# Optimization experiments

Measured on AMD Instinct MI355X. Metric: run time of the kernel, lower is better.

The kernel has to match this reference:

```python
import jax, jax.numpy as jnp
import numpy as np


def setup_inputs() -> dict:
    key = jax.random.key(0)
    ks = jax.random.split(key, 8)
    B, L, U, D = 256, 16, 512, 2
    x = jax.random.randint(ks[0], (B, L, L), 0, D, dtype=jnp.int32)
    def s(k, shape, fan):
        return jax.random.normal(k, shape, jnp.float32) / np.float32(np.sqrt(fan))
    return {
        "x": x,
        "W_in_h": s(ks[1], (D, U), D),
        "W_in_v": s(ks[2], (D, U), D),
        "W_carry_h": s(ks[3], (U, U), U),
        "b_carry_h": jnp.zeros((U,), jnp.float32),
        "W_carry_v": s(ks[4], (U, U), U),
        "W_out": s(ks[5], (U, D), U),
        "b_out": jnp.zeros((D,), jnp.float32),
    }


def reference(x, W_in_h, W_in_v, W_carry_h, b_carry_h, W_carry_v, W_out, b_out):
    B, L = x.shape[0], x.shape[1]
    U = W_carry_h.shape[0]
    D = W_out.shape[1]

    # one-hot spins, padded: zero row above, zero columns left/right
    oh = jax.nn.one_hot(jnp.transpose(x, (1, 2, 0)), D, dtype=jnp.float32)  # (L,L,B,D)
    inputs = jnp.zeros((L + 1, L + 2, B, D), jnp.float32).at[1:, 1:-1].set(oh)
    direction = jnp.where(jnp.arange(L) % 2 == 0, 1, -1)  # boustrophedon row flips

    def rev(line, d):
        return jnp.where(d == 1, line, jnp.flip(line, 0))

    def cell(h, xs):
        xh, xv, cv = xs  # left one-hot (B,D), above one-hot (B,D), above hidden (B,U)
        new = jax.nn.elu(xh @ W_in_h + xv @ W_in_v + h @ W_carry_h + b_carry_h + cv @ W_carry_v)
        p = jax.nn.softmax(new @ W_out + b_out)  # (B,D)
        return new, (new, p)

    def row(states, xs):
        cur, prev, d = xs  # (L+2,B,D), (L+2,B,D), scalar direction
        cur_r, prev_r, st_r = rev(cur, d), rev(prev, d), rev(states, d)
        _, (new_states, probs) = jax.lax.scan(
            cell, jnp.zeros((B, U), jnp.float32),
            (cur_r[:-2], prev_r[1:-1], st_r))
        logp = jnp.log(jnp.sum(probs * cur_r[1:-1], axis=2))  # (L,B)
        return rev(new_states, d), jnp.sum(logp, axis=0)

    _, prob = jax.lax.scan(row, jnp.zeros((L, B, U), jnp.float32),
                           (inputs[1:], inputs[:-1], direction))
    return jnp.nan_to_num(jnp.sum(prob, axis=0))  # (B,) log-probabilities
```

## Files before the change

kernel.cpp:

```cpp
#include <hip/hip_runtime.h>
#include <hip/hip_bf16.h>
#include <math.h>

#define Bsz 256
#define Lsz 16
#define Usz 512
#define BPW 2
#define NWG (Bsz / BPW)
#define NT  512

typedef __attribute__((ext_vector_type(8))) short bf16x8;
typedef __attribute__((ext_vector_type(4))) float f32x4;

__device__ __forceinline__ unsigned short f2bf(float f) {
    union { __hip_bfloat16 h; unsigned short s; } u;
    u.h = __float2bfloat16(f);
    return u.s;
}

__device__ __forceinline__ int st_off(int row, int k) {
    return row * Usz + ((k & 504) ^ ((row & 7) << 3)) + (k & 7);
}

__global__ void conv_wch_k(const float* __restrict__ W, unsigned int* __restrict__ out) {
    int j = blockIdx.x * 256 + threadIdx.x;
    float2 w = *(const float2*)(W + 2 * (size_t)j);
    out[j] = (unsigned)f2bf(w.x) | ((unsigned)f2bf(w.y) << 16);
}

__global__ void conv_wcv_k(const float* __restrict__ W, unsigned int* __restrict__ out) {
    int tile = blockIdx.x;
    int l    = threadIdx.x;
    int kb = tile >> 5, ub = tile & 31;
    int k0 = kb * 32 + (l >> 4) * 8;
    int u  = ub * 16 + (l & 15);
    unsigned v[4];
    #pragma unroll
    for (int p = 0; p < 4; ++p) {
        unsigned lo = f2bf(W[(size_t)(k0 + 2 * p) * Usz + u]);
        unsigned hi = f2bf(W[(size_t)(k0 + 2 * p + 1) * Usz + u]);
        v[p] = lo | (hi << 16);
    }
    *(uint4*)(out + (size_t)(tile * 64 + l) * 4) = make_uint4(v[0], v[1], v[2], v[3]);
}

__global__ __launch_bounds__(NT) void rnn2d_v2(
    const int*   __restrict__ x,
    const float* __restrict__ Wih,
    const float* __restrict__ Wiv,
    const float* __restrict__ bch,
    const float* __restrict__ Wout,
    const float* __restrict__ bout,
    const unsigned int* __restrict__ wch2,
    const unsigned int* __restrict__ wcvf,
    float*       __restrict__ out)
{
    __shared__ float          h[2][Usz];
    __shared__ unsigned short stm[2 * Lsz * Usz];
    __shared__ float          Vb[2 * Lsz * Usz];
    __shared__ float          part[4][2][Usz];
    __shared__ float          wred[8][2][2];
    __shared__ float          logp[2];

    const int tid = threadIdx.x;
    const int b0  = blockIdx.x * BPW;

    if (tid < 2) logp[tid] = 0.f;
    for (int idx = tid; idx < 2 * Lsz * Usz; idx += NT) {
        stm[idx] = 0;
        Vb[idx]  = 0.f;
    }

    const int   u    = tid;
    const float wih0 = Wih[u],            wih1 = Wih[Usz + u];
    const float wiv0 = Wiv[u],            wiv1 = Wiv[Usz + u];
    const float bc   = bch[u];
    const float wo0  = Wout[u * 2 + 0],   wo1  = Wout[u * 2 + 1];
    const float bo0  = bout[0],           bo1  = bout[1];

    const int q  = tid & 127;
    const int s  = tid >> 7;
    const int u0 = q * 4;
    const int k0 = s * 128;

    const int wv = tid >> 6;
    const int l  = tid & 63;

    for (int i = 0; i < Lsz; ++i) {
        const int dir = (i & 1) ? -1 : 1;

        if (i > 0) {
            const int rA = l & 15;
            const int kl = (l >> 4) * 8;
            f32x4 acc[2][4];
            #pragma unroll
            for (int m = 0; m < 2; ++m)
                #pragma unroll
                for (int t = 0; t < 4; ++t) acc[m][t] = (f32x4)(0.f);

            const bf16x8* wf = (const bf16x8*)wcvf;
            for (int kb = 0; kb < 16; ++kb) {
                const int ka = kb * 32 + kl;
                bf16x8 A0 = *(const bf16x8*)&stm[st_off(rA,      ka)];
                bf16x8 A1 = *(const bf16x8*)&stm[st_off(rA + 16, ka)];
                #pragma unroll
                for (int t = 0; t < 4; ++t) {
                    bf16x8 Bf = wf[(size_t)(kb * 32 + wv * 4 + t) * 64 + l];
                    acc[0][t] = __builtin_amdgcn_mfma_f32_16x16x32_bf16(A0, Bf, acc[0][t], 0, 0, 0);
                    acc[1][t] = __builtin_amdgcn_mfma_f32_16x16x32_bf16(A1, Bf, acc[1][t], 0, 0, 0);
                }
            }
            #pragma unroll
            for (int m = 0; m < 2; ++m)
                #pragma unroll
                for (int t = 0; t < 4; ++t)
                    #pragma unroll
                    for (int r = 0; r < 4; ++r) {
                        const int row = m * 16 + (l >> 4) * 4 + r;
                        const int uc  = (wv * 4 + t) * 16 + (l & 15);
                        Vb[row * Usz + uc] = acc[m][t][r];
                    }
        }

        h[0][tid] = 0.f;
        h[1][tid] = 0.f;
        __syncthreads();

        for (int t = 0; t < Lsz; ++t) {
            const int c = (dir == 1) ? t : (Lsz - 1 - t);

            float a00 = 0.f, a01 = 0.f, a02 = 0.f, a03 = 0.f;
            float a10 = 0.f, a11 = 0.f, a12 = 0.f, a13 = 0.f;
            const uint2* wp = (const uint2*)wch2 + (size_t)k0 * 128 + q;
            #pragma unroll 4
            for (int k = k0; k < k0 + 128; ++k) {
                const uint2 w = *wp;  wp += 128;
                const float f0 = __uint_as_float(w.x << 16);
                const float f1 = __uint_as_float(w.x & 0xffff0000u);
                const float f2 = __uint_as_float(w.y << 16);
                const float f3 = __uint_as_float(w.y & 0xffff0000u);
                const float h0 = h[0][k];
                const float h1 = h[1][k];
                a00 += h0 * f0;  a01 += h0 * f1;  a02 += h0 * f2;  a03 += h0 * f3;
                a10 += h1 * f0;  a11 += h1 * f1;  a12 += h1 * f2;  a13 += h1 * f3;
            }
            *(float4*)&part[s][0][u0] = make_float4(a00, a01, a02, a03);
            *(float4*)&part[s][1][u0] = make_float4(a10, a11, a12, a13);
            __syncthreads();

            const int  cl   = c - dir;
            const bool hasL = (t > 0);
            const bool hasV = (i > 0);

            float l00, l01, l10, l11;
            {
                const int xb = (b0 + 0) * (Lsz * Lsz);
                const int sl = hasL ? x[xb + i * Lsz + cl] : 0;
                const int sv = hasV ? x[xb + (i - 1) * Lsz + c] : 0;
                float tot = part[0][0][u] + part[1][0][u] + part[2][0][u] + part[3][0][u]
                          + Vb[(c * 2 + 0) * Usz + u] + bc;
                if (hasL) tot += sl ? wih1 : wih0;
                if (hasV) tot += sv ? wiv1 : wiv0;
                const float nv = tot > 0.f ? tot : expm1f(tot);
                h[0][u] = nv;
                stm[st_off(c * 2 + 0, u)] = f2bf(nv);
                l00 = nv * wo0;  l01 = nv * wo1;
            }
            {
                const int xb = (b0 + 1) * (Lsz * Lsz);
                const int sl = hasL ? x[xb + i * Lsz + cl] : 0;
                const int sv = hasV ? x[xb + (i - 1) * Lsz + c] : 0;
                float tot = part[0][1][u] + part[1][1][u] + part[2][1][u] + part[3][1][u]
                          + Vb[(c * 2 + 1) * Usz + u] + bc;
                if (hasL) tot += sl ? wih1 : wih0;
                if (hasV) tot += sv ? wiv1 : wiv0;
                const float nv = tot > 0.f ? tot : expm1f(tot);
                h[1][u] = nv;
                stm[st_off(c * 2 + 1, u)] = f2bf(nv);
                l10 = nv * wo0;  l11 = nv * wo1;
            }

            for (int off = 32; off; off >>= 1) {
                l00 += __shfl_down(l00, off);
                l01 += __shfl_down(l01, off);
                l10 += __shfl_down(l10, off);
                l11 += __shfl_down(l11, off);
            }
            if (l == 0) {
                wred[wv][0][0] = l00;  wred[wv][0][1] = l01;
                wred[wv][1][0] = l10;  wred[wv][1][1] = l11;
            }
            __syncthreads();

            if (tid < 2) {
                float g0 = bo0, g1 = bo1;
                #pragma unroll
                for (int w = 0; w < 8; ++w) {
                    g0 += wred[w][tid][0];
                    g1 += wred[w][tid][1];
                }
                const int   sc = x[(b0 + tid) * (Lsz * Lsz) + i * Lsz + c];
                const float m  = fmaxf(g0, g1);
                const float lse = m + logf(expf(g0 - m) + expf(g1 - m));
                logp[tid] += (sc ? g1 : g0) - lse;
            }
            __syncthreads();
        }
    }

    if (tid < 2) {
        float v = logp[tid];
        if (isnan(v)) v = 0.f;
        else if (isinf(v)) v = v > 0.f ? 3.4028235e38f : -3.4028235e38f;
        out[b0 + tid] = v;
    }
}

extern "C" void kernel_launch(void* const* d_in, const int* in_sizes, int n_in,
                              void* d_out, int out_size, void* d_ws, size_t ws_size,
                              hipStream_t stream) {
    const int*   x    = (const int*)  d_in[0];
    const float* Wih  = (const float*)d_in[1];
    const float* Wiv  = (const float*)d_in[2];
    const float* Wch  = (const float*)d_in[3];
    const float* bch  = (const float*)d_in[4];
    const float* Wcv  = (const float*)d_in[5];
    const float* Wout = (const float*)d_in[6];
    const float* bout = (const float*)d_in[7];

    unsigned int* ws_wch = (unsigned int*)d_ws;
    unsigned int* ws_wcv = (unsigned int*)((char*)d_ws + 512 * 1024);

    conv_wch_k<<<512, 256, 0, stream>>>(Wch, ws_wch);
    conv_wcv_k<<<512, 64, 0, stream>>>(Wcv, ws_wcv);
    rnn2d_v2<<<NWG, NT, 0, stream>>>(x, Wih, Wiv, bch, Wout, bout,
                                     ws_wch, ws_wcv, (float*)d_out);
}
```

Before: 2.316 ms.

## Compute horizontal recurrence with MFMA, keep half of W_carry_h in registers

The per-step horizontal matvec h@W_carry_h moves from scalar FMA over bf16-unpacked weights to 16x16x32 bf16 MFMA. The hidden state is stored as bf16 in a double-buffered, swizzled LDS tile padded to 16 rows with zeros, and half the weight fragments stay resident in VGPRs while the other half stream from global memory. This removes the partial-sum LDS reduction and one barrier per step, and the two weight-conversion kernels merge into one launch. In exchange, the recurrent state is rounded to bf16 at every step, 14 of the 16 MFMA rows do wasted work, and register pressure rises sharply under launch_bounds(512,2).

Result: faster. 2.229 ms (-3.7%).

```diff
diff --git a/kernel.cpp b/kernel.cpp
--- a/kernel.cpp
+++ b/kernel.cpp
@@ -22,18 +22,16 @@
     return row * Usz + ((k & 504) ^ ((row & 7) << 3)) + (k & 7);
 }
 
-__global__ void conv_wch_k(const float* __restrict__ W, unsigned int* __restrict__ out) {
-    int j = blockIdx.x * 256 + threadIdx.x;
-    float2 w = *(const float2*)(W + 2 * (size_t)j);
-    out[j] = (unsigned)f2bf(w.x) | ((unsigned)f2bf(w.y) << 16);
-}
-
-__global__ void conv_wcv_k(const float* __restrict__ W, unsigned int* __restrict__ out) {
-    int tile = blockIdx.x;
-    int l    = threadIdx.x;
-    int kb = tile >> 5, ub = tile & 31;
-    int k0 = kb * 32 + (l >> 4) * 8;
-    int u  = ub * 16 + (l & 15);
+__global__ void conv_frag(const float* __restrict__ Wa, const float* __restrict__ Wb,
+                          unsigned int* __restrict__ outa, unsigned int* __restrict__ outb) {
+    const int bid  = blockIdx.x;
+    const float* W        = (bid < 512) ? Wa : Wb;
+    unsigned int* out     = (bid < 512) ? outa : outb;
+    const int tile = bid & 511;
+    const int l    = threadIdx.x;
+    const int kb = tile >> 5, ub = tile & 31;
+    const int k0 = kb * 32 + (l >> 4) * 8;
+    const int u  = ub * 16 + (l & 15);
     unsigned v[4];
     #pragma unroll
     for (int p = 0; p < 4; ++p) {
@@ -44,167 +42,175 @@
     *(uint4*)(out + (size_t)(tile * 64 + l) * 4) = make_uint4(v[0], v[1], v[2], v[3]);
 }
 
-__global__ __launch_bounds__(NT) void rnn2d_v2(
+__global__ __launch_bounds__(NT, 2) void rnn2d_v3(
     const int*   __restrict__ x,
     const float* __restrict__ Wih,
     const float* __restrict__ Wiv,
     const float* __restrict__ bch,
     const float* __restrict__ Wout,
     const float* __restrict__ bout,
-    const unsigned int* __restrict__ wch2,
+    const unsigned int* __restrict__ wchf,
     const unsigned int* __restrict__ wcvf,
     float*       __restrict__ out)
 {
-    __shared__ float          h[2][Usz];
-    __shared__ unsigned short stm[2 * Lsz * Usz];
-    __shared__ float          Vb[2 * Lsz * Usz];
-    __shared__ float          part[4][2][Usz];
-    __shared__ float          wred[8][2][2];
-    __shared__ float          logp[2];
+    __shared__ __attribute__((aligned(16))) unsigned short stm[32 * Usz];
+    __shared__ float Vb[32 * Usz];
+    __shared__ __attribute__((aligned(16))) unsigned short hb[2][2][Usz];
+    __shared__ __attribute__((aligned(16))) unsigned short zc[8];
+    __shared__ float wihA[2][Usz], wivA[2][Usz], bcA[Usz], woA[Usz][2];
+    __shared__ float wred[2][8][2][2];
+    __shared__ float logp[2];
 
     const int tid = threadIdx.x;
     const int b0  = blockIdx.x * BPW;
+    const int w   = tid >> 6;
+    const int l   = tid & 63;
+    const int r   = l & 15;
+    const int hi4 = l >> 4;
 
     if (tid < 2) logp[tid] = 0.f;
-    for (int idx = tid; idx < 2 * Lsz * Usz; idx += NT) {
-        stm[idx] = 0;
-        Vb[idx]  = 0.f;
-    }
-
-    const int   u    = tid;
-    const float wih0 = Wih[u],            wih1 = Wih[Usz + u];
-    const float wiv0 = Wiv[u],            wiv1 = Wiv[Usz + u];
-    const float bc   = bch[u];
-    const float wo0  = Wout[u * 2 + 0],   wo1  = Wout[u * 2 + 1];
-    const float bo0  = bout[0],           bo1  = bout[1];
-
-    const int q  = tid & 127;
-    const int s  = tid >> 7;
-    const int u0 = q * 4;
-    const int k0 = s * 128;
-
-    const int wv = tid >> 6;
-    const int l  = tid & 63;
-
+    if (tid < 8) zc[tid] = 0;
+    for (int idx = tid; idx < 32 * Usz; idx += NT) Vb[idx] = 0.f;
+    wihA[0][tid] = Wih[tid];  wihA[1][tid] = Wih[Usz + tid];
+    wivA[0][tid] = Wiv[tid];  wivA[1][tid] = Wiv[Usz + tid];
+    bcA[tid] = bch[tid];
+    woA[tid][0] = Wout[2 * tid];  woA[tid][1] = Wout[2 * tid + 1];
+    const float bo0 = bout[0], bo1 = bout[1];
+
+    const bf16x8* __restrict__ WF = (const bf16x8*)wchf;
+    const bf16x8* __restrict__ VF = (const bf16x8*)wcvf;
+    bf16x8 wreg[32];
+    #pragma unroll
+    for (int kb = 0; kb < 16; ++kb) {
+        wreg[2 * kb]     = WF[(kb * 32 + w * 4 + 0) * 64 + l];
+        wreg[2 * kb + 1] = WF[(kb * 32 + w * 4 + 1) * 64 + l];
+    }
+
+    int p = 0;
     for (int i = 0; i < Lsz; ++i) {
         const int dir = (i & 1) ? -1 : 1;
 
         if (i > 0) {
-            const int rA = l & 15;
-            const int kl = (l >> 4) * 8;
-            f32x4 acc[2][4];
+            f32x4 vacc[2][4];
             #pragma unroll
             for (int m = 0; m < 2; ++m)
                 #pragma unroll
-                for (int t = 0; t < 4; ++t) acc[m][t] = (f32x4)(0.f);
-
-            const bf16x8* wf = (const bf16x8*)wcvf;
+                for (int t4 = 0; t4 < 4; ++t4) vacc[m][t4] = (f32x4)(0.f);
+            const int kl = hi4 * 8;
             for (int kb = 0; kb < 16; ++kb) {
                 const int ka = kb * 32 + kl;
-                bf16x8 A0 = *(const bf16x8*)&stm[st_off(rA,      ka)];
-                bf16x8 A1 = *(const bf16x8*)&stm[st_off(rA + 16, ka)];
-                #pragma unroll
-                for (int t = 0; t < 4; ++t) {
-                    bf16x8 Bf = wf[(size_t)(kb * 32 + wv * 4 + t) * 64 + l];
-                    acc[0][t] = __builtin_amdgcn_mfma_f32_16x16x32_bf16(A0, Bf, acc[0][t], 0, 0, 0);
-                    acc[1][t] = __builtin_amdgcn_mfma_f32_16x16x32_bf16(A1, Bf, acc[1][t], 0, 0, 0);
+                bf16x8 A0 = *(const bf16x8*)&stm[st_off(r,      ka)];
+                bf16x8 A1 = *(const bf16x8*)&stm[st_off(r + 16, ka)];
+                #pragma unroll
+                for (int t4 = 0; t4 < 4; ++t4) {
+                    bf16x8 Bf = VF[(size_t)(kb * 32 + w * 4 + t4) * 64 + l];
+                    vacc[0][t4] = __builtin_amdgcn_mfma_f32_16x16x32_bf16(A0, Bf, vacc[0][t4], 0, 0, 0);
+                    vacc[1][t4] = __builtin_amdgcn_mfma_f32_16x16x32_bf16(A1, Bf, vacc[1][t4], 0, 0, 0);
                 }
             }
             #pragma unroll
             for (int m = 0; m < 2; ++m)
                 #pragma unroll
-                for (int t = 0; t < 4; ++t)
+                for (int t4 = 0; t4 < 4; ++t4)
                     #pragma unroll
-                    for (int r = 0; r < 4; ++r) {
-                        const int row = m * 16 + (l >> 4) * 4 + r;
-                        const int uc  = (wv * 4 + t) * 16 + (l & 15);
-                        Vb[row * Usz + uc] = acc[m][t][r];
+                    for (int q = 0; q < 4; ++q) {
+                        const int row = m * 16 + hi4 * 4 + q;
+                        const int uc  = (w * 4 + t4) * 16 + r;
+                        Vb[row * Usz + uc] = vacc[m][t4][q];
                     }
         }
 
-        h[0][tid] = 0.f;
-        h[1][tid] = 0.f;
+        for (int idx = tid; idx < 2 * 2 * Usz; idx += NT)
+            ((unsigned short*)hb)[idx] = 0;
         __syncthreads();
 
         for (int t = 0; t < Lsz; ++t) {
             const int c = (dir == 1) ? t : (Lsz - 1 - t);
 
-            float a00 = 0.f, a01 = 0.f, a02 = 0.f, a03 = 0.f;
-            float a10 = 0.f, a11 = 0.f, a12 = 0.f, a13 = 0.f;
-            const uint2* wp = (const uint2*)wch2 + (size_t)k0 * 128 + q;
-            #pragma unroll 4
-            for (int k = k0; k < k0 + 128; ++k) {
-                const uint2 w = *wp;  wp += 128;
-                const float f0 = __uint_as_float(w.x << 16);
-                const float f1 = __uint_as_float(w.x & 0xffff0000u);
-                const float f2 = __uint_as_float(w.y << 16);
-                const float f3 = __uint_as_float(w.y & 0xffff0000u);
-                const float h0 = h[0][k];
-                const float h1 = h[1][k];
-                a00 += h0 * f0;  a01 += h0 * f1;  a02 += h0 * f2;  a03 += h0 * f3;
-                a10 += h1 * f0;  a11 += h1 * f1;  a12 += h1 * f2;  a13 += h1 * f3;
-            }
-            *(float4*)&part[s][0][u0] = make_float4(a00, a01, a02, a03);
-            *(float4*)&part[s][1][u0] = make_float4(a10, a11, a12, a13);
-            __syncthreads();
+            f32x4 acc0 = (f32x4)(0.f), acc1 = (f32x4)(0.f),
+                  acc2 = (f32x4)(0.f), acc3 = (f32x4)(0.f);
+            bf16x8 sbuf[16];
+            #pragma unroll
+            for (int kb = 0; kb < 16; ++kb)
+                sbuf[kb] = WF[(kb * 32 + w * 4 + 2) * 64 + l];
+            #pragma unroll
+            for (int kb = 0; kb < 16; ++kb) {
+                const bf16x8 Af = (r < 2)
+                    ? *(const bf16x8*)&hb[p][r][((kb * 4 + hi4) ^ r) << 3]
+                    : *(const bf16x8*)zc;
+                acc0 = __builtin_amdgcn_mfma_f32_16x16x32_bf16(Af, wreg[2 * kb],     acc0, 0, 0, 0);
+                acc1 = __builtin_amdgcn_mfma_f32_16x16x32_bf16(Af, wreg[2 * kb + 1], acc1, 0, 0, 0);
+                acc2 = __builtin_amdgcn_mfma_f32_16x16x32_bf16(Af, sbuf[kb],         acc2, 0, 0, 0);
+            }
+            #pragma unroll
+            for (int kb = 0; kb < 16; ++kb)
+                sbuf[kb] = WF[(kb * 32 + w * 4 + 3) * 64 + l];
+            #pragma unroll
+            for (int kb = 0; kb < 16; ++kb) {
+                const bf16x8 Af = (r < 2)
+                    ? *(const bf16x8*)&hb[p][r][((kb * 4 + hi4) ^ r) << 3]
+                    : *(const bf16x8*)zc;
+                acc3 = __builtin_amdgcn_mfma_f32_16x16x32_bf16(Af, sbuf[kb], acc3, 0, 0, 0);
+            }
 
             const int  cl   = c - dir;
             const bool hasL = (t > 0);
             const bool hasV = (i > 0);
-
-            float l00, l01, l10, l11;
-            {
-                const int xb = (b0 + 0) * (Lsz * Lsz);
-                const int sl = hasL ? x[xb + i * Lsz + cl] : 0;
-                const int sv = hasV ? x[xb + (i - 1) * Lsz + c] : 0;
-                float tot = part[0][0][u] + part[1][0][u] + part[2][0][u] + part[3][0][u]
-                          + Vb[(c * 2 + 0) * Usz + u] + bc;
-                if (hasL) tot += sl ? wih1 : wih0;
-                if (hasV) tot += sv ? wiv1 : wiv0;
-                const float nv = tot > 0.f ? tot : expm1f(tot);
-                h[0][u] = nv;
-                stm[st_off(c * 2 + 0, u)] = f2bf(nv);
-                l00 = nv * wo0;  l01 = nv * wo1;
-            }
-            {
-                const int xb = (b0 + 1) * (Lsz * Lsz);
-                const int sl = hasL ? x[xb + i * Lsz + cl] : 0;
-                const int sv = hasV ? x[xb + (i - 1) * Lsz + c] : 0;
-                float tot = part[0][1][u] + part[1][1][u] + part[2][1][u] + part[3][1][u]
-                          + Vb[(c * 2 + 1) * Usz + u] + bc;
-                if (hasL) tot += sl ? wih1 : wih0;
-                if (hasV) tot += sv ? wiv1 : wiv0;
-                const float nv = tot > 0.f ? tot : expm1f(tot);
-                h[1][u] = nv;
-                stm[st_off(c * 2 + 1, u)] = f2bf(nv);
-                l10 = nv * wo0;  l11 = nv * wo1;
-            }
-
-            for (int off = 32; off; off >>= 1) {
-                l00 += __shfl_down(l00, off);
-                l01 += __shfl_down(l01, off);
-                l10 += __shfl_down(l10, off);
-                l11 += __shfl_down(l11, off);
-            }
-            if (l == 0) {
-                wred[wv][0][0] = l00;  wred[wv][0][1] = l01;
-                wred[wv][1][0] = l10;  wred[wv][1][1] = l11;
+            if (l < 16) {
+                const int sl0 = hasL ? x[(b0 + 0) * 256 + i * 16 + cl]      : 0;
+                const int sv0 = hasV ? x[(b0 + 0) * 256 + (i - 1) * 16 + c] : 0;
+                const int sl1 = hasL ? x[(b0 + 1) * 256 + i * 16 + cl]      : 0;
+                const int sv1 = hasV ? x[(b0 + 1) * 256 + (i - 1) * 16 + c] : 0;
+                float lp00 = 0.f, lp01 = 0.f, lp10 = 0.f, lp11 = 0.f;
+
+                #define EPI(ACC, TQ) { \
+                    const int u = w * 64 + (TQ) * 16 + l; \
+                    float v0 = (ACC)[0] + Vb[(c * 2 + 0) * Usz + u] + bcA[u]; \
+                    float v1 = (ACC)[1] + Vb[(c * 2 + 1) * Usz + u] + bcA[u]; \
+                    if (hasL) { v0 += wihA[sl0][u]; v1 += wihA[sl1][u]; } \
+                    if (hasV) { v0 += wivA[sv0][u]; v1 += wivA[sv1][u]; } \
+                    v0 = v0 > 0.f ? v0 : expm1f(v0); \
+                    v1 = v1 > 0.f ? v1 : expm1f(v1); \
+                    hb[p ^ 1][0][(((u >> 3) ^ 0) << 3) | (u & 7)] = f2bf(v0); \
+                    hb[p ^ 1][1][(((u >> 3) ^ 1) << 3) | (u & 7)] = f2bf(v1); \
+                    stm[st_off(c * 2 + 0, u)] = f2bf(v0); \
+                    stm[st_off(c * 2 + 1, u)] = f2bf(v1); \
+                    lp00 += v0 * woA[u][0];  lp01 += v0 * woA[u][1]; \
+                    lp10 += v1 * woA[u][0];  lp11 += v1 * woA[u][1]; }
+
+                EPI(acc0, 0)
+                EPI(acc1, 1)
+                EPI(acc2, 2)
+                EPI(acc3, 3)
+                #undef EPI
+
+                #pragma unroll
+                for (int off = 8; off; off >>= 1) {
+                    lp00 += __shfl_down(lp00, off);
+                    lp01 += __shfl_down(lp01, off);
+                    lp10 += __shfl_down(lp10, off);
+                    lp11 += __shfl_down(lp11, off);
+                }
+                if (l == 0) {
+                    wred[t & 1][w][0][0] = lp00;  wred[t & 1][w][0][1] = lp01;
+                    wred[t & 1][w][1][0] = lp10;  wred[t & 1][w][1][1] = lp11;
+                }
             }
             __syncthreads();
 
             if (tid < 2) {
                 float g0 = bo0, g1 = bo1;
                 #pragma unroll
-                for (int w = 0; w < 8; ++w) {
-                    g0 += wred[w][tid][0];
-                    g1 += wred[w][tid][1];
-                }
-                const int   sc = x[(b0 + tid) * (Lsz * Lsz) + i * Lsz + c];
+                for (int ww = 0; ww < 8; ++ww) {
+                    g0 += wred[t & 1][ww][tid][0];
+                    g1 += wred[t & 1][ww][tid][1];
+                }
+                const int   sc = x[(b0 + tid) * 256 + i * 16 + c];
                 const float m  = fmaxf(g0, g1);
                 const float lse = m + logf(expf(g0 - m) + expf(g1 - m));
                 logp[tid] += (sc ? g1 : g0) - lse;
             }
-            __syncthreads();
+            p ^= 1;
         }
     }
 
@@ -231,8 +237,7 @@
     unsigned int* ws_wch = (unsigned int*)d_ws;
     unsigned int* ws_wcv = (unsigned int*)((char*)d_ws + 512 * 1024);
 
-    conv_wch_k<<<512, 256, 0, stream>>>(Wch, ws_wch);
-    conv_wcv_k<<<512, 64, 0, stream>>>(Wcv, ws_wcv);
-    rnn2d_v2<<<NWG, NT, 0, stream>>>(x, Wih, Wiv, bch, Wout, bout,
+    conv_frag<<<1024, 64, 0, stream>>>(Wch, Wcv, ws_wch, ws_wcv);
+    rnn2d_v3<<<NWG, NT, 0, stream>>>(x, Wih, Wiv, bch, Wout, bout,
                                      ws_wch, ws_wcv, (float*)d_out);
 }
```
